# Performance work log

Hardware: AMD Instinct MI355X
Metric: run time of the kernel (lower is better)

Reference implementation:

```python
import jax, jax.numpy as jnp
import numpy as np
from jax.ops import segment_sum

N_NODES = 50000
N_EDGES = 800000
HIDDEN = 96
N_CLASSES = 10
N_GRAPHS = 64


def gcn_conv(x, W, b, src, dst, num_nodes):
    """PyG GCNConv: symmetric-normalized aggregation with self-loops.
    out = D^{-1/2} (A + I) D^{-1/2} (x W) + b, with D the degree of A + I.
    Self-loop contribution handled analytically instead of appending edges.
    """
    ones = jnp.ones((src.shape[0],), dtype=x.dtype)
    deg = segment_sum(ones, dst, num_segments=num_nodes) + 1.0  # +1 for self-loop
    dinv = jax.lax.rsqrt(deg)
    h = x @ W  # [N, H] small GEMM
    norm = dinv[src] * dinv[dst]  # [E]
    msg = h[src] * norm[:, None]  # [E, H] dominant gather
    out = segment_sum(msg, dst, num_segments=num_nodes)  # scatter-add
    out = out + h * (dinv * dinv)[:, None]  # self-loop term
    return out + b


def setup_inputs() -> dict:
    key = jax.random.key(0)
    ks = jax.random.split(key, 12)
    x = jax.random.normal(ks[0], (N_NODES, HIDDEN), dtype=jnp.float32)
    edge_index = jax.random.randint(ks[1], (2, N_EDGES), 0, N_NODES, dtype=jnp.int64)
    batch = jnp.sort(jax.random.randint(ks[2], (N_NODES,), 0, N_GRAPHS, dtype=jnp.int64))
    s = 1.0 / np.sqrt(HIDDEN)
    W0 = jax.random.normal(ks[3], (HIDDEN, HIDDEN), dtype=jnp.float32) * s
    b0 = jnp.zeros((HIDDEN,), dtype=jnp.float32)
    W1 = jax.random.normal(ks[4], (HIDDEN, HIDDEN), dtype=jnp.float32) * s
    b1 = jnp.zeros((HIDDEN,), dtype=jnp.float32)
    W2 = jax.random.normal(ks[5], (HIDDEN, HIDDEN), dtype=jnp.float32) * s
    b2 = jnp.zeros((HIDDEN,), dtype=jnp.float32)
    W_lin = jax.random.normal(ks[6], (HIDDEN, N_CLASSES), dtype=jnp.float32) * s
    b_lin = jnp.zeros((N_CLASSES,), dtype=jnp.float32)
    return {"x": x, "edge_index": edge_index, "batch": batch,
            "W0": W0, "b0": b0, "W1": W1, "b1": b1, "W2": W2, "b2": b2,
            "W_lin": W_lin, "b_lin": b_lin}


def reference(x, edge_index, batch, W0, b0, W1, b1, W2, b2, W_lin, b_lin):
    src, dst = edge_index[0], edge_index[1]
    n = x.shape[0]
    h = jax.nn.relu(gcn_conv(x, W0, b0, src, dst, n))
    h = jax.nn.relu(gcn_conv(h, W1, b1, src, dst, n))
    h = gcn_conv(h, W2, b2, src, dst, n)  # last layer: no activation
    # global_mean_pool over batch index
    sums = segment_sum(h, batch, num_segments=N_GRAPHS)  # [G, H]
    cnts = segment_sum(jnp.ones((n,), dtype=h.dtype), batch, num_segments=N_GRAPHS)
    pooled = sums / jnp.maximum(cnts, 1.0)[:, None]
    # dropout is identity in eval mode
    return pooled @ W_lin + b_lin  # [G, num_classes]
```

## Files before the change

kernel.cpp:

```cpp
#include <hip/hip_runtime.h>
#include <hip/hip_bf16.h>

#define HID 96
#define NGRAPHS 64
#define SENT 0xC3C3u
#define NROWS 50116

typedef __attribute__((ext_vector_type(8))) short short8;
typedef __attribute__((ext_vector_type(4))) float floatx4;
typedef __attribute__((ext_vector_type(2))) float floatx2;
typedef __attribute__((ext_vector_type(8))) unsigned short ushort8v;
typedef __attribute__((ext_vector_type(2))) unsigned int uint2v;

__device__ __forceinline__ float bf16_to_f32(unsigned short u) {
    unsigned int v = ((unsigned int)u) << 16;
    return __builtin_bit_cast(float, v);
}
__device__ __forceinline__ unsigned short f32_to_bf16(float f) {
    unsigned int u = __builtin_bit_cast(unsigned int, f);
    u += 0x7fff + ((u >> 16) & 1);
    return (unsigned short)(u >> 16);
}
__device__ __forceinline__ unsigned char f32_to_fp8(float f) {
    return (unsigned char)(__builtin_amdgcn_cvt_pk_fp8_f32(f, f, 0, false) & 0xff);
}
__device__ __forceinline__ uint2v f32x8_to_fp8(const float* v) {
    int lo = 0, hi = 0;
    lo = __builtin_amdgcn_cvt_pk_fp8_f32(v[0], v[1], lo, false);
    lo = __builtin_amdgcn_cvt_pk_fp8_f32(v[2], v[3], lo, true);
    hi = __builtin_amdgcn_cvt_pk_fp8_f32(v[4], v[5], hi, false);
    hi = __builtin_amdgcn_cvt_pk_fp8_f32(v[6], v[7], hi, true);
    uint2v r;
    r[0] = (unsigned int)lo;
    r[1] = (unsigned int)hi;
    return r;
}

__device__ __forceinline__ void gather_core8(
    const unsigned char* __restrict__ h8, const unsigned short* __restrict__ csr,
    int r0, int r1, int r2, int TAIL, int it2, int pe8,
    float* __restrict__ aA, float* __restrict__ aB) {
    int s = r0;
    ushort8v i0 = *(const ushort8v*)(csr + (s < r2 ? s : TAIL));
    ushort8v i1 = *(const ushort8v*)(csr + (s + 8 < r2 ? s + 8 : TAIL));
    for (int it = 0; it < it2; ++it) {
        uint2v v0[8], v1[8];
#pragma unroll
        for (int j = 0; j < 8; ++j)
            v0[j] = *(const uint2v*)(h8 + (int)i0[j] * HID + pe8);
#pragma unroll
        for (int j = 0; j < 8; ++j)
            v1[j] = *(const uint2v*)(h8 + (int)i1[j] * HID + pe8);
        int sn = s + 16;
        ushort8v n0 = *(const ushort8v*)(csr + (sn < r2 ? sn : TAIL));
        ushort8v n1 = *(const ushort8v*)(csr + (sn + 8 < r2 ? sn + 8 : TAIL));
        bool cA0 = s < r1;
        bool cA1 = (s + 8) < r1;
        float t0[8] = {0, 0, 0, 0, 0, 0, 0, 0};
        float t1[8] = {0, 0, 0, 0, 0, 0, 0, 0};
#pragma unroll
        for (int j = 0; j < 8; ++j) {
            floatx2 a0 = __builtin_amdgcn_cvt_pk_f32_fp8(v0[j][0], false);
            floatx2 a1 = __builtin_amdgcn_cvt_pk_f32_fp8(v0[j][0], true);
            floatx2 a2 = __builtin_amdgcn_cvt_pk_f32_fp8(v0[j][1], false);
            floatx2 a3 = __builtin_amdgcn_cvt_pk_f32_fp8(v0[j][1], true);
            t0[0] += a0[0]; t0[1] += a0[1]; t0[2] += a1[0]; t0[3] += a1[1];
            t0[4] += a2[0]; t0[5] += a2[1]; t0[6] += a3[0]; t0[7] += a3[1];
        }
#pragma unroll
        for (int j = 0; j < 8; ++j) {
            floatx2 b0 = __builtin_amdgcn_cvt_pk_f32_fp8(v1[j][0], false);
            floatx2 b1 = __builtin_amdgcn_cvt_pk_f32_fp8(v1[j][0], true);
            floatx2 b2 = __builtin_amdgcn_cvt_pk_f32_fp8(v1[j][1], false);
            floatx2 b3 = __builtin_amdgcn_cvt_pk_f32_fp8(v1[j][1], true);
            t1[0] += b0[0]; t1[1] += b0[1]; t1[2] += b1[0]; t1[3] += b1[1];
            t1[4] += b2[0]; t1[5] += b2[1]; t1[6] += b3[0]; t1[7] += b3[1];
        }
#pragma unroll
        for (int f = 0; f < 8; ++f) {
            float x0 = cA0 ? t0[f] : 0.0f;
            aA[f] += x0;
            aB[f] += t0[f] - x0;
            float x1 = cA1 ? t1[f] : 0.0f;
            aA[f] += x1;
            aB[f] += t1[f] - x1;
        }
        i0 = n0;
        i1 = n1;
        s = sn;
    }
}

__device__ __forceinline__ void fp8x8_decode(uint2v u, float* __restrict__ o) {
    floatx2 a0 = __builtin_amdgcn_cvt_pk_f32_fp8(u[0], false);
    floatx2 a1 = __builtin_amdgcn_cvt_pk_f32_fp8(u[0], true);
    floatx2 a2 = __builtin_amdgcn_cvt_pk_f32_fp8(u[1], false);
    floatx2 a3 = __builtin_amdgcn_cvt_pk_f32_fp8(u[1], true);
    o[0] = a0[0]; o[1] = a0[1]; o[2] = a1[0]; o[3] = a1[1];
    o[4] = a2[0]; o[5] = a2[1]; o[6] = a3[0]; o[7] = a3[1];
}

__global__ __launch_bounds__(256) void init_kernel(
    int* __restrict__ deg, float* __restrict__ psum,
    unsigned char* __restrict__ bufA, unsigned char* __restrict__ bufB, int N,
    int NB, const float* __restrict__ W0, const float* __restrict__ W1,
    const float* __restrict__ W2, unsigned short* __restrict__ Wz) {
    int b = blockIdx.x;
    if (b >= NB) {
        int wsel = b - NB;
        const float* W = (wsel == 0) ? W0 : (wsel == 1) ? W1 : W2;
        unsigned short* dst = Wz + wsel * HID * HID;
        for (int e = threadIdx.x; e < HID * HID; e += blockDim.x) {
            int k = e / HID, n = e % HID;
            int nt = n >> 4, kki = k >> 5, quad = (k >> 3) & 3, j = k & 7;
            int lane = (n & 15) | (quad << 4);
            dst[(((nt * 3 + kki) * 64 + lane) << 3) | j] = f32_to_bf16(W[e]);
        }
        return;
    }
    int i = b * 256 + threadIdx.x;
    if (i < N) deg[i] = 0;
    if (i < NGRAPHS * HID + NGRAPHS) psum[i] = 0.0f;
    if (i < HID) {
        bufA[(size_t)SENT * HID + i] = 0;
        bufB[(size_t)SENT * HID + i] = 0;
    }
}

__global__ void deg_kernel(const int* __restrict__ dst, int* __restrict__ deg,
                           int n_edges) {
    int t = blockIdx.x * blockDim.x + threadIdx.x;
    int e0 = t * 4;
    if (e0 + 4 <= n_edges) {
        int4 d4 = *(const int4*)(dst + e0);
        atomicAdd(&deg[d4.x], 1);
        atomicAdd(&deg[d4.y], 1);
        atomicAdd(&deg[d4.z], 1);
        atomicAdd(&deg[d4.w], 1);
    } else {
        for (int e = e0; e < n_edges; e++) atomicAdd(&deg[dst[e]], 1);
    }
}

__global__ __launch_bounds__(256) void scan_phaseA(const int* __restrict__ deg,
                                                   float* __restrict__ dinv,
                                                   int* __restrict__ blocksum,
                                                   int N) {
    int i = blockIdx.x * 256 + threadIdx.x;
    int d = (i < N) ? deg[i] : 0;
    if (i < N) dinv[i] = rsqrtf((float)d + 1.0f);
    int v = (d + 7) & ~7;
#pragma unroll
    for (int off = 32; off > 0; off >>= 1) v += __shfl_down(v, off, 64);
    __shared__ int s[4];
    if ((threadIdx.x & 63) == 0) s[threadIdx.x >> 6] = v;
    __syncthreads();
    if (threadIdx.x == 0) blocksum[blockIdx.x] = s[0] + s[1] + s[2] + s[3];
}

__global__ __launch_bounds__(256) void scan_phaseC(const int* __restrict__ deg,
                                                   const int* __restrict__ blocksum,
                                                   int* __restrict__ rowptr,
                                                   int* __restrict__ cursor,
                                                   int N, int NB) {
    int t = threadIdx.x;
    int mine = (t < NB && t < blockIdx.x) ? blocksum[t] : 0;
#pragma unroll
    for (int off = 32; off > 0; off >>= 1) mine += __shfl_down(mine, off, 64);
    __shared__ int ps[4];
    if ((t & 63) == 0) ps[t >> 6] = mine;
    __syncthreads();
    int pref = ps[0] + ps[1] + ps[2] + ps[3];

    __shared__ int s[256];
    int i = blockIdx.x * 256 + t;
    int own = (i < N) ? (deg[i] + 7) & ~7 : 0;
    s[t] = own;
    __syncthreads();
#pragma unroll
    for (int off = 1; off < 256; off <<= 1) {
        int v = (t >= off) ? s[t - off] : 0;
        __syncthreads();
        s[t] += v;
        __syncthreads();
    }
    if (i < N) {
        int r = pref + s[t] - own;
        rowptr[i] = r;
        cursor[i] = r;
        if (i == N - 1) rowptr[N] = r + own;
    }
}

__global__ void csr_fill(const int* __restrict__ src, const int* __restrict__ dst,
                         int* __restrict__ cursor,
                         unsigned short* __restrict__ csr_src, int n_edges) {
    int t = blockIdx.x * blockDim.x + threadIdx.x;
    int e0 = t * 8;
    if (e0 + 8 <= n_edges) {
        int4 da = *(const int4*)(dst + e0);
        int4 db = *(const int4*)(dst + e0 + 4);
        int4 sa = *(const int4*)(src + e0);
        int4 sb = *(const int4*)(src + e0 + 4);
        int p0 = atomicAdd(&cursor[da.x], 1);
        int p1 = atomicAdd(&cursor[da.y], 1);
        int p2 = atomicAdd(&cursor[da.z], 1);
        int p3 = atomicAdd(&cursor[da.w], 1);
        int p4 = atomicAdd(&cursor[db.x], 1);
        int p5 = atomicAdd(&cursor[db.y], 1);
        int p6 = atomicAdd(&cursor[db.z], 1);
        int p7 = atomicAdd(&cursor[db.w], 1);
        csr_src[p0] = (unsigned short)sa.x;
        csr_src[p1] = (unsigned short)sa.y;
        csr_src[p2] = (unsigned short)sa.z;
        csr_src[p3] = (unsigned short)sa.w;
        csr_src[p4] = (unsigned short)sb.x;
        csr_src[p5] = (unsigned short)sb.y;
        csr_src[p6] = (unsigned short)sb.z;
        csr_src[p7] = (unsigned short)sb.w;
    } else {
        for (int e = e0; e < n_edges; e++) {
            int p = atomicAdd(&cursor[dst[e]], 1);
            csr_src[p] = (unsigned short)src[e];
        }
    }
}

__global__ __launch_bounds__(256) void gemm0_f32(
    const float* __restrict__ X, const unsigned short* __restrict__ Wz,
    const float* __restrict__ dinv, unsigned char* __restrict__ Out, int Mtiles) {
    int wv = threadIdx.x >> 6;
    int lane = threadIdx.x & 63;
    int quad = lane >> 4;
    int mrow = lane & 15;
    int tt = blockIdx.x * 2 + (wv >> 1);
    int half = wv & 1;
    if (tt >= Mtiles) return;

    short8 bfrag[9];
    const short8* Wz8 = (const short8*)Wz;
#pragma unroll
    for (int f = 0; f < 9; f++) bfrag[f] = Wz8[(half * 9 + f) * 64 + lane];

    int m0 = tt * 16;
    const float* arow = X + (size_t)(m0 + mrow) * HID + quad * 8;
    short8 a[3];
#pragma unroll
    for (int kb = 0; kb < 3; kb++) {
        float4 u = *(const float4*)(arow + kb * 32);
        float4 v = *(const float4*)(arow + kb * 32 + 4);
        short8 t;
        t[0] = (short)f32_to_bf16(u.x); t[1] = (short)f32_to_bf16(u.y);
        t[2] = (short)f32_to_bf16(u.z); t[3] = (short)f32_to_bf16(u.w);
        t[4] = (short)f32_to_bf16(v.x); t[5] = (short)f32_to_bf16(v.y);
        t[6] = (short)f32_to_bf16(v.z); t[7] = (short)f32_to_bf16(v.w);
        a[kb] = t;
    }
    float dscale[4];
#pragma unroll
    for (int r = 0; r < 4; r++) dscale[r] = dinv[m0 + quad * 4 + r];
    unsigned char* orow = Out + (size_t)m0 * HID;
#pragma unroll
    for (int ntl = 0; ntl < 3; ntl++) {
        int nt = half * 3 + ntl;
        floatx4 c = {0.0f, 0.0f, 0.0f, 0.0f};
        c = __builtin_amdgcn_mfma_f32_16x16x32_bf16(a[0], bfrag[ntl * 3 + 0], c, 0, 0, 0);
        c = __builtin_amdgcn_mfma_f32_16x16x32_bf16(a[1], bfrag[ntl * 3 + 1], c, 0, 0, 0);
        c = __builtin_amdgcn_mfma_f32_16x16x32_bf16(a[2], bfrag[ntl * 3 + 2], c, 0, 0, 0);
#pragma unroll
        for (int r = 0; r < 4; r++)
            orow[(size_t)(quad * 4 + r) * HID + nt * 16 + mrow] =
                f32_to_fp8(c[r] * dscale[r]);
    }
}

__global__ __launch_bounds__(256) void fused_gather_gemm(
    const unsigned char* __restrict__ h8, const int* __restrict__ rowptr,
    const unsigned short* __restrict__ csr, const float* __restrict__ dinv,
    const float* __restrict__ bias, const unsigned short* __restrict__ Wz,
    unsigned char* __restrict__ Out, int Mtiles, int N) {
    __shared__ unsigned short tile[2][16][104];
    int wv = threadIdx.x >> 6;
    int lane = threadIdx.x & 63;
    int quad = lane >> 4;
    int mrow = lane & 15;
    int tsel = wv >> 1;
    int half = wv & 1;
    int tt = blockIdx.x * 2 + tsel;
    bool active = tt < Mtiles;
    int g = lane >> 4;
    int p = lane & 15;
    int pe = (p < 12) ? p : 11;
    int pe8 = pe * 8;

    if (active) {
        int TAIL = rowptr[N];
        int j0 = half * 8 + g * 2;
        int na = tt * 16 + j0;
        int r0 = rowptr[na], r1 = rowptr[na + 1], r2 = rowptr[na + 2];
        float da = dinv[na], db = dinv[na + 1];
        float aA[8], aB[8];
        uint2v sva = *(const uint2v*)(h8 + (size_t)na * HID + pe8);
        uint2v svb = *(const uint2v*)(h8 + (size_t)(na + 1) * HID + pe8);
        fp8x8_decode(sva, aA);
        fp8x8_decode(svb, aB);
        int it2 = (r2 - r0 + 15) >> 4;
        int o = __shfl_xor(it2, 16, 64);
        it2 = it2 > o ? it2 : o;
        o = __shfl_xor(it2, 32, 64);
        it2 = it2 > o ? it2 : o;
        gather_core8(h8, csr, r0, r1, r2, TAIL, it2, pe8, aA, aB);
        float4 bb0 = *(const float4*)(bias + pe8);
        float4 bb1 = *(const float4*)(bias + pe8 + 4);
        float bv[8] = {bb0.x, bb0.y, bb0.z, bb0.w, bb1.x, bb1.y, bb1.z, bb1.w};
        if (p < 12) {
            ushort8v oA, oB;
#pragma unroll
            for (int f = 0; f < 8; ++f) {
                oA[f] = f32_to_bf16(fmaxf(aA[f] * da + bv[f], 0.0f));
                oB[f] = f32_to_bf16(fmaxf(aB[f] * db + bv[f], 0.0f));
            }
            *(ushort8v*)(&tile[tsel][j0][pe8]) = oA;
            *(ushort8v*)(&tile[tsel][j0 + 1][pe8]) = oB;
        }
    }
    __syncthreads();
    if (!active) return;

    short8 bfrag[9];
    const short8* Wz8 = (const short8*)Wz;
#pragma unroll
    for (int f = 0; f < 9; f++) bfrag[f] = Wz8[(half * 9 + f) * 64 + lane];

    const unsigned short* tp = &tile[tsel][0][0];
    short8 a[3];
#pragma unroll
    for (int kb = 0; kb < 3; kb++)
        a[kb] = *(const short8*)(tp + mrow * 104 + quad * 8 + kb * 32);
    int n0 = tt * 16;
    float dscale[4];
#pragma unroll
    for (int r = 0; r < 4; r++) dscale[r] = dinv[n0 + quad * 4 + r];
    unsigned char* orow = Out + (size_t)n0 * HID;
#pragma unroll
    for (int ntl = 0; ntl < 3; ntl++) {
        int nt = half * 3 + ntl;
        floatx4 c = {0.0f, 0.0f, 0.0f, 0.0f};
        c = __builtin_amdgcn_mfma_f32_16x16x32_bf16(a[0], bfrag[ntl * 3 + 0], c, 0, 0, 0);
        c = __builtin_amdgcn_mfma_f32_16x16x32_bf16(a[1], bfrag[ntl * 3 + 1], c, 0, 0, 0);
        c = __builtin_amdgcn_mfma_f32_16x16x32_bf16(a[2], bfrag[ntl * 3 + 2], c, 0, 0, 0);
#pragma unroll
        for (int r = 0; r < 4; r++)
            orow[(size_t)(quad * 4 + r) * HID + nt * 16 + mrow] =
                f32_to_fp8(c[r] * dscale[r]);
    }
}

__global__ __launch_bounds__(256) void gather_pool(
    const unsigned char* __restrict__ h8, const int* __restrict__ rowptr,
    const unsigned short* __restrict__ csr, const float* __restrict__ dinv,
    const float* __restrict__ bias, const int* __restrict__ batch,
    float* __restrict__ psum, float* __restrict__ pcnt, int Ntiles8, int N) {
    __shared__ float stage[4][8][96];
    int wv = threadIdx.x >> 6;
    int lane = threadIdx.x & 63;
    int tt = blockIdx.x * 4 + wv;
    if (tt >= Ntiles8) return;
    int g = lane >> 4;
    int p = lane & 15;
    int pe = (p < 12) ? p : 11;
    int pe8 = pe * 8;

    int TAIL = rowptr[N];
    int n0 = tt * 8;
    int na = n0 + g * 2;
    int r0 = rowptr[na], r1 = rowptr[na + 1], r2 = rowptr[na + 2];
    float da = dinv[na], db = dinv[na + 1];
    float aA[8], aB[8];
    uint2v sva = *(const uint2v*)(h8 + (size_t)na * HID + pe8);
    uint2v svb = *(const uint2v*)(h8 + (size_t)(na + 1) * HID + pe8);
    fp8x8_decode(sva, aA);
    fp8x8_decode(svb, aB);
    int it2 = (r2 - r0 + 15) >> 4;
    int o = __shfl_xor(it2, 16, 64);
    it2 = it2 > o ? it2 : o;
    o = __shfl_xor(it2, 32, 64);
    it2 = it2 > o ? it2 : o;
    gather_core8(h8, csr, r0, r1, r2, TAIL, it2, pe8, aA, aB);
    float4 bb0 = *(const float4*)(bias + pe8);
    float4 bb1 = *(const float4*)(bias + pe8 + 4);
    float bv[8] = {bb0.x, bb0.y, bb0.z, bb0.w, bb1.x, bb1.y, bb1.z, bb1.w};
    if (p < 12) {
        floatx4 oa0 = {aA[0] * da + bv[0], aA[1] * da + bv[1],
                       aA[2] * da + bv[2], aA[3] * da + bv[3]};
        floatx4 oa1 = {aA[4] * da + bv[4], aA[5] * da + bv[5],
                       aA[6] * da + bv[6], aA[7] * da + bv[7]};
        floatx4 ob0 = {aB[0] * db + bv[0], aB[1] * db + bv[1],
                       aB[2] * db + bv[2], aB[3] * db + bv[3]};
        floatx4 ob1 = {aB[4] * db + bv[4], aB[5] * db + bv[5],
                       aB[6] * db + bv[6], aB[7] * db + bv[7]};
        *(floatx4*)(&stage[wv][g * 2][pe8]) = oa0;
        *(floatx4*)(&stage[wv][g * 2][pe8 + 4]) = oa1;
        *(floatx4*)(&stage[wv][g * 2 + 1][pe8]) = ob0;
        *(floatx4*)(&stage[wv][g * 2 + 1][pe8 + 4]) = ob1;
    }
    asm volatile("s_waitcnt lgkmcnt(0)" ::: "memory");

    int fi = (lane < 48) ? lane * 2 : 94;
    int g_cur = batch[n0];
    float s0 = 0.0f, s1 = 0.0f;
    int cnt = 0;
#pragma unroll
    for (int j = 0; j < 8; ++j) {
        int gb = batch[n0 + j];
        if (gb != g_cur) {
            if (lane < 48) {
                atomicAdd(&psum[g_cur * HID + fi], s0);
                atomicAdd(&psum[g_cur * HID + fi + 1], s1);
            }
            if (lane == 0) atomicAdd(&pcnt[g_cur], (float)cnt);
            s0 = 0.0f; s1 = 0.0f; cnt = 0;
            g_cur = gb;
        }
        s0 += stage[wv][j][fi];
        s1 += stage[wv][j][fi + 1];
        cnt++;
    }
    if (lane < 48) {
        atomicAdd(&psum[g_cur * HID + fi], s0);
        atomicAdd(&psum[g_cur * HID + fi + 1], s1);
    }
    if (lane == 0) atomicAdd(&pcnt[g_cur], (float)cnt);
}

__global__ __launch_bounds__(640) void final_kernel(
    const float* __restrict__ sums, const float* __restrict__ cnts,
    const float* __restrict__ Wlin, const float* __restrict__ blin,
    float* __restrict__ out) {
    int t = threadIdx.x;
    if (t >= NGRAPHS * 10) return;
    int g = t / 10;
    int c = t % 10;
    float denom = fmaxf(cnts[g], 1.0f);
    float acc = blin[c];
#pragma unroll
    for (int f = 0; f < HID; f++)
        acc += (sums[g * HID + f] / denom) * Wlin[f * 10 + c];
    out[t] = acc;
}

extern "C" void kernel_launch(void* const* d_in, const int* in_sizes, int n_in,
                              void* d_out, int out_size, void* d_ws,
                              size_t ws_size, hipStream_t stream) {
    const float* x = (const float*)d_in[0];
    const int* edge = (const int*)d_in[1];
    const int* batch = (const int*)d_in[2];
    const float* W[3] = {(const float*)d_in[3], (const float*)d_in[5],
                         (const float*)d_in[7]};
    const float* B[3] = {(const float*)d_in[4], (const float*)d_in[6],
                         (const float*)d_in[8]};
    const float* Wlin = (const float*)d_in[9];
    const float* blin = (const float*)d_in[10];
    float* out = (float*)d_out;

    int N = in_sizes[0] / HID;
    int E = in_sizes[1] / 2;
    const int* src = edge;
    const int* dst = edge + E;
    int NB = (N + 255) / 256;

    char* ws = (char*)d_ws;
    size_t off = 0;
    auto alloc = [&](size_t bytes) {
        void* p = ws + off;
        off += (bytes + 255) & ~(size_t)255;
        return p;
    };
    int* deg = (int*)alloc((size_t)N * 4);
    float* dinv = (float*)alloc((size_t)N * 4);
    int* rowptr = (int*)alloc(((size_t)N + 1) * 4);
    int* cursor = (int*)alloc((size_t)N * 4);
    int* blocksum = (int*)alloc((size_t)NB * 4);
    size_t csr_cap = (size_t)E + 8 * (size_t)N;
    unsigned short* csr_src = (unsigned short*)alloc(csr_cap * 2 + 64);
    unsigned short* Wz = (unsigned short*)alloc(3 * HID * HID * 2);
    unsigned char* bufA = (unsigned char*)alloc((size_t)NROWS * HID);
    unsigned char* bufB = (unsigned char*)alloc((size_t)NROWS * HID);
    float* psum = (float*)alloc((NGRAPHS * HID + NGRAPHS) * 4);
    float* pcnt = psum + NGRAPHS * HID;

    hipMemsetAsync(csr_src, 0xC3, csr_cap * 2, stream);
    init_kernel<<<NB + 3, 256, 0, stream>>>(deg, psum, bufA, bufB, N, NB,
                                            W[0], W[1], W[2], Wz);
    deg_kernel<<<(E / 4 + 255) / 256, 256, 0, stream>>>(dst, deg, E);
    scan_phaseA<<<NB, 256, 0, stream>>>(deg, dinv, blocksum, N);
    scan_phaseC<<<NB, 256, 0, stream>>>(deg, blocksum, rowptr, cursor, N, NB);
    csr_fill<<<(E / 8 + 255) / 256, 256, 0, stream>>>(src, dst, cursor, csr_src, E);

    int Mtiles = (N + 15) / 16;
    int grid2 = (Mtiles + 1) / 2;
    int Ntiles8 = (N + 7) / 8;
    int gridp = (Ntiles8 + 3) / 4;

    gemm0_f32<<<grid2, 256, 0, stream>>>(x, Wz, dinv, bufA, Mtiles);
    fused_gather_gemm<<<grid2, 256, 0, stream>>>(
        bufA, rowptr, csr_src, dinv, B[0], Wz + 1 * HID * HID, bufB, Mtiles, N);
    fused_gather_gemm<<<grid2, 256, 0, stream>>>(
        bufB, rowptr, csr_src, dinv, B[1], Wz + 2 * HID * HID, bufA, Mtiles, N);
    gather_pool<<<gridp, 256, 0, stream>>>(bufA, rowptr, csr_src, dinv, B[2],
                                           batch, psum, pcnt, Ntiles8, N);
    final_kernel<<<1, 640, 0, stream>>>(psum, pcnt, Wlin, blin, out);
}
```

Baseline: 302.8 us.

## Split fp8 feature buffer into two 48-column planes and gather per plane

Stores the fp8 hidden features as two column planes of 48 bytes per row instead of one 96-byte row. The gather now runs twice, once per plane, with each 16-lane group split into two 8-lane halves that take alternate edges, and the halves are combined with a cross-lane shuffle. The aim is a smaller per-pass working set that fits cache better, with 6 of 8 lanes active instead of 12 of 16. The cost is a second pass over the CSR indices, extra shuffles, and more loop iterations per node.

```diff
diff --git a/kernel.cpp b/kernel.cpp
--- a/kernel.cpp
+++ b/kernel.cpp
@@ -5,6 +5,7 @@
 #define NGRAPHS 64
 #define SENT 0xC3C3u
 #define NROWS 50116
+#define PLN ((size_t)NROWS * 48)
 
 typedef __attribute__((ext_vector_type(8))) short short8;
 typedef __attribute__((ext_vector_type(4))) float floatx4;
@@ -24,73 +25,6 @@
 __device__ __forceinline__ unsigned char f32_to_fp8(float f) {
     return (unsigned char)(__builtin_amdgcn_cvt_pk_fp8_f32(f, f, 0, false) & 0xff);
 }
-__device__ __forceinline__ uint2v f32x8_to_fp8(const float* v) {
-    int lo = 0, hi = 0;
-    lo = __builtin_amdgcn_cvt_pk_fp8_f32(v[0], v[1], lo, false);
-    lo = __builtin_amdgcn_cvt_pk_fp8_f32(v[2], v[3], lo, true);
-    hi = __builtin_amdgcn_cvt_pk_fp8_f32(v[4], v[5], hi, false);
-    hi = __builtin_amdgcn_cvt_pk_fp8_f32(v[6], v[7], hi, true);
-    uint2v r;
-    r[0] = (unsigned int)lo;
-    r[1] = (unsigned int)hi;
-    return r;
-}
-
-__device__ __forceinline__ void gather_core8(
-    const unsigned char* __restrict__ h8, const unsigned short* __restrict__ csr,
-    int r0, int r1, int r2, int TAIL, int it2, int pe8,
-    float* __restrict__ aA, float* __restrict__ aB) {
-    int s = r0;
-    ushort8v i0 = *(const ushort8v*)(csr + (s < r2 ? s : TAIL));
-    ushort8v i1 = *(const ushort8v*)(csr + (s + 8 < r2 ? s + 8 : TAIL));
-    for (int it = 0; it < it2; ++it) {
-        uint2v v0[8], v1[8];
-#pragma unroll
-        for (int j = 0; j < 8; ++j)
-            v0[j] = *(const uint2v*)(h8 + (int)i0[j] * HID + pe8);
-#pragma unroll
-        for (int j = 0; j < 8; ++j)
-            v1[j] = *(const uint2v*)(h8 + (int)i1[j] * HID + pe8);
-        int sn = s + 16;
-        ushort8v n0 = *(const ushort8v*)(csr + (sn < r2 ? sn : TAIL));
-        ushort8v n1 = *(const ushort8v*)(csr + (sn + 8 < r2 ? sn + 8 : TAIL));
-        bool cA0 = s < r1;
-        bool cA1 = (s + 8) < r1;
-        float t0[8] = {0, 0, 0, 0, 0, 0, 0, 0};
-        float t1[8] = {0, 0, 0, 0, 0, 0, 0, 0};
-#pragma unroll
-        for (int j = 0; j < 8; ++j) {
-            floatx2 a0 = __builtin_amdgcn_cvt_pk_f32_fp8(v0[j][0], false);
-            floatx2 a1 = __builtin_amdgcn_cvt_pk_f32_fp8(v0[j][0], true);
-            floatx2 a2 = __builtin_amdgcn_cvt_pk_f32_fp8(v0[j][1], false);
-            floatx2 a3 = __builtin_amdgcn_cvt_pk_f32_fp8(v0[j][1], true);
-            t0[0] += a0[0]; t0[1] += a0[1]; t0[2] += a1[0]; t0[3] += a1[1];
-            t0[4] += a2[0]; t0[5] += a2[1]; t0[6] += a3[0]; t0[7] += a3[1];
-        }
-#pragma unroll
-        for (int j = 0; j < 8; ++j) {
-            floatx2 b0 = __builtin_amdgcn_cvt_pk_f32_fp8(v1[j][0], false);
-            floatx2 b1 = __builtin_amdgcn_cvt_pk_f32_fp8(v1[j][0], true);
-            floatx2 b2 = __builtin_amdgcn_cvt_pk_f32_fp8(v1[j][1], false);
-            floatx2 b3 = __builtin_amdgcn_cvt_pk_f32_fp8(v1[j][1], true);
-            t1[0] += b0[0]; t1[1] += b0[1]; t1[2] += b1[0]; t1[3] += b1[1];
-            t1[4] += b2[0]; t1[5] += b2[1]; t1[6] += b3[0]; t1[7] += b3[1];
-        }
-#pragma unroll
-        for (int f = 0; f < 8; ++f) {
-            float x0 = cA0 ? t0[f] : 0.0f;
-            aA[f] += x0;
-            aB[f] += t0[f] - x0;
-            float x1 = cA1 ? t1[f] : 0.0f;
-            aA[f] += x1;
-            aB[f] += t1[f] - x1;
-        }
-        i0 = n0;
-        i1 = n1;
-        s = sn;
-    }
-}
-
 __device__ __forceinline__ void fp8x8_decode(uint2v u, float* __restrict__ o) {
     floatx2 a0 = __builtin_amdgcn_cvt_pk_f32_fp8(u[0], false);
     floatx2 a1 = __builtin_amdgcn_cvt_pk_f32_fp8(u[0], true);
@@ -98,6 +32,54 @@
     floatx2 a3 = __builtin_amdgcn_cvt_pk_f32_fp8(u[1], true);
     o[0] = a0[0]; o[1] = a0[1]; o[2] = a1[0]; o[3] = a1[1];
     o[4] = a2[0]; o[5] = a2[1]; o[6] = a3[0]; o[7] = a3[1];
+}
+
+__device__ __forceinline__ void gather_half(
+    const unsigned char* __restrict__ hp, const unsigned short* __restrict__ csr,
+    int r0, int r1, int r2, int TAIL, int it2, int sub, int il8e,
+    float* __restrict__ aA, float* __restrict__ aB) {
+    int s = r0;
+    ushort8v i0 = *(const ushort8v*)(csr + (s < r2 ? s : TAIL));
+    ushort8v i1 = *(const ushort8v*)(csr + (s + 8 < r2 ? s + 8 : TAIL));
+    for (int it = 0; it < it2; ++it) {
+        uint2v v0[4], v1[4];
+#pragma unroll
+        for (int k = 0; k < 4; ++k)
+            v0[k] = *(const uint2v*)(hp + (int)i0[2 * k + sub] * 48 + il8e);
+#pragma unroll
+        for (int k = 0; k < 4; ++k)
+            v1[k] = *(const uint2v*)(hp + (int)i1[2 * k + sub] * 48 + il8e);
+        int sn = s + 16;
+        ushort8v n0 = *(const ushort8v*)(csr + (sn < r2 ? sn : TAIL));
+        ushort8v n1 = *(const ushort8v*)(csr + (sn + 8 < r2 ? sn + 8 : TAIL));
+#pragma unroll
+        for (int k = 0; k < 4; ++k) {
+            float t[8];
+            fp8x8_decode(v0[k], t);
+            bool cA = (s + 2 * k + sub) < r1;
+#pragma unroll
+            for (int f = 0; f < 8; ++f) {
+                float x = cA ? t[f] : 0.0f;
+                aA[f] += x;
+                aB[f] += t[f] - x;
+            }
+        }
+#pragma unroll
+        for (int k = 0; k < 4; ++k) {
+            float t[8];
+            fp8x8_decode(v1[k], t);
+            bool cA = (s + 8 + 2 * k + sub) < r1;
+#pragma unroll
+            for (int f = 0; f < 8; ++f) {
+                float x = cA ? t[f] : 0.0f;
+                aA[f] += x;
+                aB[f] += t[f] - x;
+            }
+        }
+        i0 = n0;
+        i1 = n1;
+        s = sn;
+    }
 }
 
 __global__ __launch_bounds__(256) void init_kernel(
@@ -121,9 +103,11 @@
     int i = b * 256 + threadIdx.x;
     if (i < N) deg[i] = 0;
     if (i < NGRAPHS * HID + NGRAPHS) psum[i] = 0.0f;
-    if (i < HID) {
-        bufA[(size_t)SENT * HID + i] = 0;
-        bufB[(size_t)SENT * HID + i] = 0;
+    if (i < 48) {
+        bufA[(size_t)SENT * 48 + i] = 0;
+        bufA[PLN + (size_t)SENT * 48 + i] = 0;
+        bufB[(size_t)SENT * 48 + i] = 0;
+        bufB[PLN + (size_t)SENT * 48 + i] = 0;
     }
 }
 
@@ -259,17 +243,16 @@
     float dscale[4];
 #pragma unroll
     for (int r = 0; r < 4; r++) dscale[r] = dinv[m0 + quad * 4 + r];
-    unsigned char* orow = Out + (size_t)m0 * HID;
+    unsigned char* op = Out + (size_t)half * PLN + (size_t)m0 * 48;
 #pragma unroll
     for (int ntl = 0; ntl < 3; ntl++) {
-        int nt = half * 3 + ntl;
         floatx4 c = {0.0f, 0.0f, 0.0f, 0.0f};
         c = __builtin_amdgcn_mfma_f32_16x16x32_bf16(a[0], bfrag[ntl * 3 + 0], c, 0, 0, 0);
         c = __builtin_amdgcn_mfma_f32_16x16x32_bf16(a[1], bfrag[ntl * 3 + 1], c, 0, 0, 0);
         c = __builtin_amdgcn_mfma_f32_16x16x32_bf16(a[2], bfrag[ntl * 3 + 2], c, 0, 0, 0);
 #pragma unroll
         for (int r = 0; r < 4; r++)
-            orow[(size_t)(quad * 4 + r) * HID + nt * 16 + mrow] =
+            op[(size_t)(quad * 4 + r) * 48 + ntl * 16 + mrow] =
                 f32_to_fp8(c[r] * dscale[r]);
     }
 }
@@ -289,9 +272,9 @@
     int tt = blockIdx.x * 2 + tsel;
     bool active = tt < Mtiles;
     int g = lane >> 4;
-    int p = lane & 15;
-    int pe = (p < 12) ? p : 11;
-    int pe8 = pe * 8;
+    int sub = (lane & 15) >> 3;
+    int il = lane & 7;
+    int il8e = (il < 6 ? il : 5) * 8;
 
     if (active) {
         int TAIL = rowptr[N];
@@ -299,29 +282,46 @@
         int na = tt * 16 + j0;
         int r0 = rowptr[na], r1 = rowptr[na + 1], r2 = rowptr[na + 2];
         float da = dinv[na], db = dinv[na + 1];
-        float aA[8], aB[8];
-        uint2v sva = *(const uint2v*)(h8 + (size_t)na * HID + pe8);
-        uint2v svb = *(const uint2v*)(h8 + (size_t)(na + 1) * HID + pe8);
-        fp8x8_decode(sva, aA);
-        fp8x8_decode(svb, aB);
         int it2 = (r2 - r0 + 15) >> 4;
         int o = __shfl_xor(it2, 16, 64);
         it2 = it2 > o ? it2 : o;
         o = __shfl_xor(it2, 32, 64);
         it2 = it2 > o ? it2 : o;
-        gather_core8(h8, csr, r0, r1, r2, TAIL, it2, pe8, aA, aB);
-        float4 bb0 = *(const float4*)(bias + pe8);
-        float4 bb1 = *(const float4*)(bias + pe8 + 4);
-        float bv[8] = {bb0.x, bb0.y, bb0.z, bb0.w, bb1.x, bb1.y, bb1.z, bb1.w};
-        if (p < 12) {
-            ushort8v oA, oB;
+#pragma unroll 1
+        for (int ph = 0; ph < 2; ++ph) {
+            const unsigned char* hp = h8 + (size_t)ph * PLN;
+            uint2v sva = *(const uint2v*)(hp + (size_t)na * 48 + il8e);
+            uint2v svb = *(const uint2v*)(hp + (size_t)(na + 1) * 48 + il8e);
+            float aA[8] = {0, 0, 0, 0, 0, 0, 0, 0};
+            float aB[8] = {0, 0, 0, 0, 0, 0, 0, 0};
+            gather_half(hp, csr, r0, r1, r2, TAIL, it2, sub, il8e, aA, aB);
 #pragma unroll
             for (int f = 0; f < 8; ++f) {
-                oA[f] = f32_to_bf16(fmaxf(aA[f] * da + bv[f], 0.0f));
-                oB[f] = f32_to_bf16(fmaxf(aB[f] * db + bv[f], 0.0f));
+                aA[f] += __shfl_xor(aA[f], 8, 64);
+                aB[f] += __shfl_xor(aB[f], 8, 64);
             }
-            *(ushort8v*)(&tile[tsel][j0][pe8]) = oA;
-            *(ushort8v*)(&tile[tsel][j0 + 1][pe8]) = oB;
+            float sA[8], sB[8];
+            fp8x8_decode(sva, sA);
+            fp8x8_decode(svb, sB);
+#pragma unroll
+            for (int f = 0; f < 8; ++f) {
+                aA[f] += sA[f];
+                aB[f] += sB[f];
+            }
+            const float* bp = bias + ph * 48 + il8e;
+            float4 bb0 = *(const float4*)(bp);
+            float4 bb1 = *(const float4*)(bp + 4);
+            float bv[8] = {bb0.x, bb0.y, bb0.z, bb0.w, bb1.x, bb1.y, bb1.z, bb1.w};
+            if ((lane & 15) < 6) {
+                ushort8v oA, oB;
+#pragma unroll
+                for (int f = 0; f < 8; ++f) {
+                    oA[f] = f32_to_bf16(fmaxf(aA[f] * da + bv[f], 0.0f));
+                    oB[f] = f32_to_bf16(fmaxf(aB[f] * db + bv[f], 0.0f));
+                }
+                *(ushort8v*)(&tile[tsel][j0][ph * 48 + il8e]) = oA;
+                *(ushort8v*)(&tile[tsel][j0 + 1][ph * 48 + il8e]) = oB;
+            }
         }
     }
     __syncthreads();
@@ -341,17 +341,16 @@
     float dscale[4];
 #pragma unroll
     for (int r = 0; r < 4; r++) dscale[r] = dinv[n0 + quad * 4 + r];
-    unsigned char* orow = Out + (size_t)n0 * HID;
+    unsigned char* op = Out + (size_t)half * PLN + (size_t)n0 * 48;
 #pragma unroll
     for (int ntl = 0; ntl < 3; ntl++) {
-        int nt = half * 3 + ntl;
         floatx4 c = {0.0f, 0.0f, 0.0f, 0.0f};
         c = __builtin_amdgcn_mfma_f32_16x16x32_bf16(a[0], bfrag[ntl * 3 + 0], c, 0, 0, 0);
         c = __builtin_amdgcn_mfma_f32_16x16x32_bf16(a[1], bfrag[ntl * 3 + 1], c, 0, 0, 0);
         c = __builtin_amdgcn_mfma_f32_16x16x32_bf16(a[2], bfrag[ntl * 3 + 2], c, 0, 0, 0);
 #pragma unroll
         for (int r = 0; r < 4; r++)
-            orow[(size_t)(quad * 4 + r) * HID + nt * 16 + mrow] =
+            op[(size_t)(quad * 4 + r) * 48 + ntl * 16 + mrow] =
                 f32_to_fp8(c[r] * dscale[r]);
     }
 }
@@ -367,42 +366,60 @@
     int tt = blockIdx.x * 4 + wv;
     if (tt >= Ntiles8) return;
     int g = lane >> 4;
-    int p = lane & 15;
-    int pe = (p < 12) ? p : 11;
-    int pe8 = pe * 8;
+    int sub = (lane & 15) >> 3;
+    int il = lane & 7;
+    int il8e = (il < 6 ? il : 5) * 8;
 
     int TAIL = rowptr[N];
     int n0 = tt * 8;
     int na = n0 + g * 2;
     int r0 = rowptr[na], r1 = rowptr[na + 1], r2 = rowptr[na + 2];
     float da = dinv[na], db = dinv[na + 1];
-    float aA[8], aB[8];
-    uint2v sva = *(const uint2v*)(h8 + (size_t)na * HID + pe8);
-    uint2v svb = *(const uint2v*)(h8 + (size_t)(na + 1) * HID + pe8);
-    fp8x8_decode(sva, aA);
-    fp8x8_decode(svb, aB);
     int it2 = (r2 - r0 + 15) >> 4;
     int o = __shfl_xor(it2, 16, 64);
     it2 = it2 > o ? it2 : o;
     o = __shfl_xor(it2, 32, 64);
     it2 = it2 > o ? it2 : o;
-    gather_core8(h8, csr, r0, r1, r2, TAIL, it2, pe8, aA, aB);
-    float4 bb0 = *(const float4*)(bias + pe8);
-    float4 bb1 = *(const float4*)(bias + pe8 + 4);
-    float bv[8] = {bb0.x, bb0.y, bb0.z, bb0.w, bb1.x, bb1.y, bb1.z, bb1.w};
-    if (p < 12) {
-        floatx4 oa0 = {aA[0] * da + bv[0], aA[1] * da + bv[1],
-                       aA[2] * da + bv[2], aA[3] * da + bv[3]};
-        floatx4 oa1 = {aA[4] * da + bv[4], aA[5] * da + bv[5],
-                       aA[6] * da + bv[6], aA[7] * da + bv[7]};
-        floatx4 ob0 = {aB[0] * db + bv[0], aB[1] * db + bv[1],
-                       aB[2] * db + bv[2], aB[3] * db + bv[3]};
-        floatx4 ob1 = {aB[4] * db + bv[4], aB[5] * db + bv[5],
-                       aB[6] * db + bv[6], aB[7] * db + bv[7]};
-        *(floatx4*)(&stage[wv][g * 2][pe8]) = oa0;
-        *(floatx4*)(&stage[wv][g * 2][pe8 + 4]) = oa1;
-        *(floatx4*)(&stage[wv][g * 2 + 1][pe8]) = ob0;
-        *(floatx4*)(&stage[wv][g * 2 + 1][pe8 + 4]) = ob1;
+#pragma unroll 1
+    for (int ph = 0; ph < 2; ++ph) {
+        const unsigned char* hp = h8 + (size_t)ph * PLN;
+        uint2v sva = *(const uint2v*)(hp + (size_t)na * 48 + il8e);
+        uint2v svb = *(const uint2v*)(hp + (size_t)(na + 1) * 48 + il8e);
+        float aA[8] = {0, 0, 0, 0, 0, 0, 0, 0};
+        float aB[8] = {0, 0, 0, 0, 0, 0, 0, 0};
+        gather_half(hp, csr, r0, r1, r2, TAIL, it2, sub, il8e, aA, aB);
+#pragma unroll
+        for (int f = 0; f < 8; ++f) {
+            aA[f] += __shfl_xor(aA[f], 8, 64);
+            aB[f] += __shfl_xor(aB[f], 8, 64);
+        }
+        float sA[8], sB[8];
+        fp8x8_decode(sva, sA);
+        fp8x8_decode(svb, sB);
+#pragma unroll
+        for (int f = 0; f < 8; ++f) {
+            aA[f] += sA[f];
+            aB[f] += sB[f];
+        }
+        const float* bp = bias + ph * 48 + il8e;
+        float4 bb0 = *(const float4*)(bp);
+        float4 bb1 = *(const float4*)(bp + 4);
+        float bv[8] = {bb0.x, bb0.y, bb0.z, bb0.w, bb1.x, bb1.y, bb1.z, bb1.w};
+        if ((lane & 15) < 6) {
+            floatx4 oa0 = {aA[0] * da + bv[0], aA[1] * da + bv[1],
+                           aA[2] * da + bv[2], aA[3] * da + bv[3]};
+            floatx4 oa1 = {aA[4] * da + bv[4], aA[5] * da + bv[5],
+                           aA[6] * da + bv[6], aA[7] * da + bv[7]};
+            floatx4 ob0 = {aB[0] * db + bv[0], aB[1] * db + bv[1],
+                           aB[2] * db + bv[2], aB[3] * db + bv[3]};
+            floatx4 ob1 = {aB[4] * db + bv[4], aB[5] * db + bv[5],
+                           aB[6] * db + bv[6], aB[7] * db + bv[7]};
+            int col = ph * 48 + il8e;
+            *(floatx4*)(&stage[wv][g * 2][col]) = oa0;
+            *(floatx4*)(&stage[wv][g * 2][col + 4]) = oa1;
+            *(floatx4*)(&stage[wv][g * 2 + 1][col]) = ob0;
+            *(floatx4*)(&stage[wv][g * 2 + 1][col + 4]) = ob1;
+        }
     }
     asm volatile("s_waitcnt lgkmcnt(0)" ::: "memory");
 
@@ -484,8 +501,8 @@
     size_t csr_cap = (size_t)E + 8 * (size_t)N;
     unsigned short* csr_src = (unsigned short*)alloc(csr_cap * 2 + 64);
     unsigned short* Wz = (unsigned short*)alloc(3 * HID * HID * 2);
-    unsigned char* bufA = (unsigned char*)alloc((size_t)NROWS * HID);
-    unsigned char* bufB = (unsigned char*)alloc((size_t)NROWS * HID);
+    unsigned char* bufA = (unsigned char*)alloc(2 * PLN);
+    unsigned char* bufB = (unsigned char*)alloc(2 * PLN);
     float* psum = (float*)alloc((NGRAPHS * HID + NGRAPHS) * 4);
     float* pcnt = psum + NGRAPHS * HID;
 
```

Result: slower. 355.1 us (+17.3%).
